# Kernel tuning notes

Measured on AMD Instinct MI355X. Metric: run time of the kernel, lower is better.

The kernel has to match this reference:

```python
import jax, jax.numpy as jnp
import numpy as np

HEADS = 16
KV_HEADS = 4
DIM_HEAD = 128
DIM = 2048
ROPE_BASE = 10000.0


def rotate_half(t):
    t1, t2 = jnp.split(t, 2, axis=-1)
    return jnp.concatenate((-t2, t1), axis=-1)


def apply_rotary(t, cos, sin):
    # t: [b, h, n, d]; cos/sin: [n, d]
    return t * cos + rotate_half(t) * sin


def setup_inputs() -> dict:
    key = jax.random.key(0)
    ks = jax.random.split(key, 6)
    b, n = 4, 1024
    s = 1.0 / np.sqrt(DIM)
    x = jax.random.normal(ks[0], (b, n, DIM), dtype=jnp.float32)
    Wq = jax.random.normal(ks[1], (DIM, HEADS * DIM_HEAD), dtype=jnp.float32) * s
    Wk = jax.random.normal(ks[2], (DIM, KV_HEADS * DIM_HEAD), dtype=jnp.float32) * s
    Wv = jax.random.normal(ks[3], (DIM, KV_HEADS * DIM_HEAD), dtype=jnp.float32) * s
    Wo = jax.random.normal(ks[4], (HEADS * DIM_HEAD, DIM), dtype=jnp.float32) * s
    head_scale = 1.0 + 0.02 * jax.random.normal(ks[5], (1, HEADS, 1, 1), dtype=jnp.float32)
    return {"x": x, "Wq": Wq, "Wk": Wk, "Wv": Wv, "Wo": Wo, "head_scale": head_scale}


def reference(x, Wq, Wk, Wv, Wo, head_scale):
    b, n, _ = x.shape
    # projections
    q = (x @ Wq).reshape(b, n, HEADS, DIM_HEAD).transpose(0, 2, 1, 3)      # b h n d
    k = (x @ Wk).reshape(b, n, KV_HEADS, DIM_HEAD).transpose(0, 2, 1, 3)   # b kv n d
    v = (x @ Wv).reshape(b, n, KV_HEADS, DIM_HEAD).transpose(0, 2, 1, 3)
    # rotary embeddings
    inv_freq = 1.0 / (ROPE_BASE ** (jnp.arange(0, DIM_HEAD, 2, dtype=jnp.float32) / DIM_HEAD))
    freqs = jnp.arange(n, dtype=jnp.float32)[:, None] * inv_freq[None, :]  # n, d/2
    emb = jnp.concatenate((freqs, freqs), axis=-1)                          # n, d
    cos, sin = jnp.cos(emb), jnp.sin(emb)
    q = apply_rotary(q, cos, sin)
    k = apply_rotary(k, cos, sin)
    # GQA: expand kv heads to query heads
    rep = HEADS // KV_HEADS
    k = jnp.repeat(k, rep, axis=1)
    v = jnp.repeat(v, rep, axis=1)
    # attention with causal mask
    scale = 1.0 / jnp.sqrt(jnp.array(DIM_HEAD, dtype=x.dtype))
    scores = jnp.einsum('bhid,bhjd->bhij', q, k) * scale
    causal = jnp.tril(jnp.ones((n, n), dtype=bool))
    scores = jnp.where(causal, scores, jnp.finfo(scores.dtype).min)
    attn = jax.nn.softmax(scores, axis=-1)
    out = jnp.einsum('bhij,bhjd->bhid', attn, v)
    out = out * head_scale                                                  # learned per-head scale
    out = out.transpose(0, 2, 1, 3).reshape(b, n, HEADS * DIM_HEAD)
    return out @ Wo
```

## Files before the change

kernel.cpp:

```cpp
#include <hip/hip_runtime.h>

typedef __attribute__((ext_vector_type(8))) short short8;
typedef __attribute__((ext_vector_type(8), may_alias)) short short8a;
typedef __attribute__((ext_vector_type(4))) short short4a_ __attribute__((may_alias));
typedef __attribute__((ext_vector_type(4))) float float4_;
typedef __attribute__((ext_vector_type(4), may_alias)) float float4a;

__device__ __forceinline__ float b2f(short h) {
  unsigned int u = ((unsigned int)(unsigned short)h) << 16;
  return __builtin_bit_cast(float, u);
}
__device__ __forceinline__ short f2b(float f) {
  unsigned int u = __builtin_bit_cast(unsigned int, f);
  u += 0x7fffu + ((u >> 16) & 1u);
  return (short)(unsigned short)(u >> 16);
}

#define GLOBAL_AS __attribute__((address_space(1)))
#define LDS_AS    __attribute__((address_space(3)))
__device__ __forceinline__ void async_copy16(void* lds, const void* g) {
  __builtin_amdgcn_global_load_lds((GLOBAL_AS const void*)g, (LDS_AS void*)lds, 16, 0, 0);
}

__global__ __launch_bounds__(256) void prep(const float* __restrict__ x,
                                            const float* __restrict__ Wq,
                                            const float* __restrict__ Wk,
                                            const float* __restrict__ Wv,
                                            const float* __restrict__ Wo,
                                            short* __restrict__ xb,
                                            short* __restrict__ wqkvt,
                                            short* __restrict__ wot) {
  __shared__ float tile[64][65];
  int bid = blockIdx.x;
  if (bid < 1536) {
    int k0 = (bid & 31) * 64, n0 = (bid >> 5) * 64;
    for (int idx = threadIdx.x; idx < 4096; idx += 256) {
      int r = idx >> 6, cc = idx & 63;
      int n = n0 + cc;
      float v;
      if (n < 2048)      v = Wq[(size_t)(k0 + r) * 2048 + n];
      else if (n < 2560) v = Wk[(size_t)(k0 + r) * 512 + (n - 2048)];
      else               v = Wv[(size_t)(k0 + r) * 512 + (n - 2560)];
      tile[r][cc] = v;
    }
    __syncthreads();
    for (int idx = threadIdx.x; idx < 4096; idx += 256) {
      int r = idx >> 6, cc = idx & 63;
      wqkvt[(size_t)(n0 + r) * 2048 + k0 + cc] = f2b(tile[cc][r]);
    }
  } else if (bid < 2560) {
    int t = bid - 1536;
    int k0 = (t & 31) * 64, n0 = (t >> 5) * 64;
    for (int idx = threadIdx.x; idx < 4096; idx += 256) {
      int r = idx >> 6, cc = idx & 63;
      tile[r][cc] = Wo[(size_t)(k0 + r) * 2048 + n0 + cc];
    }
    __syncthreads();
    for (int idx = threadIdx.x; idx < 4096; idx += 256) {
      int r = idx >> 6, cc = idx & 63;
      wot[(size_t)(n0 + r) * 2048 + k0 + cc] = f2b(tile[cc][r]);
    }
  } else {
    int i = (bid - 2560) * 256 + threadIdx.x;
    float4a v = ((const float4a*)x)[i];
    short4a_ o;
    o.x = f2b(v.x); o.y = f2b(v.y); o.z = f2b(v.z); o.w = f2b(v.w);
    ((short4a_*)xb)[i] = o;
  }
}

template <bool BF16OUT>
__global__ __launch_bounds__(256, 2)
void gemm_bt(const short* __restrict__ A, const short* __restrict__ B,
             void* __restrict__ Cv, int M, int N, int K) {
  __shared__ alignas(16) short lA[128 * 64];
  __shared__ alignas(16) short lB[128 * 64];
  const int tid = threadIdx.x;
  const int wave = tid >> 6, lane = tid & 63;
  const int quad = lane >> 4, l16 = lane & 15;
  const int m0 = blockIdx.x * 128, n0 = blockIdx.y * 128;
  const int wm = (wave >> 1) * 64, wn = (wave & 1) * 64;
  float4_ acc[4][4];
#pragma unroll
  for (int i = 0; i < 4; i++)
#pragma unroll
    for (int j = 0; j < 4; j++) acc[i][j] = (float4_){0.f, 0.f, 0.f, 0.f};
  const int nK = K >> 6;
  const int srow = lane >> 3, slot = lane & 7;
  for (int kt = 0; kt < nK; ++kt) {
    __syncthreads();
#pragma unroll
    for (int cth = 0; cth < 4; ++cth) {
      int rb = wave * 32 + cth * 8;
      int r = rb + srow;
      int c = slot ^ (r & 7);
      async_copy16(&lA[rb * 64], A + (size_t)(m0 + r) * K + kt * 64 + c * 8);
      async_copy16(&lB[rb * 64], B + (size_t)(n0 + r) * K + kt * 64 + c * 8);
    }
    __syncthreads();
#pragma unroll
    for (int kc = 0; kc < 2; ++kc) {
      short8 af[4], bf[4];
      int cch = kc * 4 + quad;
#pragma unroll
      for (int mt = 0; mt < 4; ++mt) {
        int ar = wm + mt * 16 + l16;
        af[mt] = *(const short8a*)&lA[ar * 64 + (cch ^ (ar & 7)) * 8];
      }
#pragma unroll
      for (int nt = 0; nt < 4; ++nt) {
        int br = wn + nt * 16 + l16;
        bf[nt] = *(const short8a*)&lB[br * 64 + (cch ^ (br & 7)) * 8];
      }
#pragma unroll
      for (int mt = 0; mt < 4; ++mt)
#pragma unroll
        for (int nt = 0; nt < 4; ++nt)
          acc[mt][nt] = __builtin_amdgcn_mfma_f32_16x16x32_bf16(af[mt], bf[nt], acc[mt][nt], 0, 0, 0);
    }
  }
#pragma unroll
  for (int mt = 0; mt < 4; ++mt)
#pragma unroll
    for (int nt = 0; nt < 4; ++nt) {
      int row = m0 + wm + mt * 16 + quad * 4;
      int col = n0 + wn + nt * 16 + l16;
      float4_ v = acc[mt][nt];
      if (BF16OUT) {
        short* Cb = (short*)Cv;
#pragma unroll
        for (int r = 0; r < 4; r++) Cb[(size_t)(row + r) * N + col] = f2b(v[r]);
      } else {
        float* Cf = (float*)Cv;
#pragma unroll
        for (int r = 0; r < 4; r++) Cf[(size_t)(row + r) * N + col] = v[r];
      }
    }
}

__global__ __launch_bounds__(256) void rope(short* __restrict__ qkv) {
  __shared__ float cs[64], sn[64];
  int row = blockIdx.x;
  int pos = row & 1023;
  if (threadIdx.x < 64) {
    float inv = exp2f((float)threadIdx.x * -0.20762050593478f);
    float a = (float)pos * inv;
    cs[threadIdx.x] = cosf(a);
    sn[threadIdx.x] = sinf(a);
  }
  __syncthreads();
  short* p = qkv + (size_t)row * 3072;
  for (int t = threadIdx.x; t < 1280; t += 256) {
    int hh = t >> 6, i = t & 63;
    int base = (hh < 16) ? hh * 128 : 2048 + (hh - 16) * 128;
    float scl = (hh < 16) ? 0.08838834764831845f : 1.0f;
    float c = cs[i], s = sn[i];
    float t1 = b2f(p[base + i]), t2 = b2f(p[base + 64 + i]);
    p[base + i]      = f2b((t1 * c - t2 * s) * scl);
    p[base + 64 + i] = f2b((t2 * c + t1 * s) * scl);
  }
}

__global__ __launch_bounds__(256) void vt_build(const short* __restrict__ qkv, short* __restrict__ vt) {
  __shared__ short tile[128][65];
  int bkv = blockIdx.x, n0 = blockIdx.y * 64;
  int b = bkv >> 2, kv = bkv & 3;
  const short* src = qkv + (size_t)(b * 1024) * 3072 + 2560 + kv * 128;
#pragma unroll
  for (int it = 0; it < 4; ++it) {
    int n = it * 16 + (threadIdx.x >> 4), ch = threadIdx.x & 15;
    short8a v = *(const short8a*)(src + (size_t)(n0 + n) * 3072 + ch * 8);
#pragma unroll
    for (int j = 0; j < 8; ++j) tile[ch * 8 + j][n] = v[j];
  }
  __syncthreads();
#pragma unroll
  for (int it = 0; it < 4; ++it) {
    int idx = it * 256 + threadIdx.x;
    int d = idx >> 3, ch = idx & 7;
    short8a v;
#pragma unroll
    for (int j = 0; j < 8; ++j) v[j] = tile[d][ch * 8 + j];
    *(short8a*)(vt + (size_t)(bkv * 128 + d) * 1024 + n0 + ch * 8) = v;
  }
}

__global__ __launch_bounds__(256, 2)
void flash(const short* __restrict__ qkv, const short* __restrict__ vt,
           const float* __restrict__ head_scale, short* __restrict__ attn) {
  __shared__ alignas(16) short lK[64 * 128];
  __shared__ alignas(16) short lV[128 * 64];
  __shared__ alignas(16) short lP[4][16 * 72];
  const int tid = threadIdx.x, wave = tid >> 6, lane = tid & 63;
  const int quad = lane >> 4, l16 = lane & 15;
  const int bh = blockIdx.x, b = bh >> 4, h = bh & 15, kv = h >> 2;
  const int qt = (gridDim.y - 1) - blockIdx.y;
  short8 qf[4];
  {
    int qrow = qt * 64 + wave * 16 + l16;
    const short* qp = qkv + (size_t)(b * 1024 + qrow) * 3072 + h * 128;
#pragma unroll
    for (int kc = 0; kc < 4; kc++) qf[kc] = *(const short8a*)(qp + kc * 32 + quad * 8);
  }
  float4_ O[8];
#pragma unroll
  for (int i = 0; i < 8; i++) O[i] = (float4_){0.f, 0.f, 0.f, 0.f};
  float rsacc[4] = {0.f, 0.f, 0.f, 0.f};
  const size_t kbase = (size_t)(b * 1024) * 3072 + 2048 + kv * 128;
  const size_t vbase = (size_t)((b * 4 + kv) * 128) * 1024;
  const int slot16 = lane & 15, rr4 = lane >> 4;
  const int slot8 = lane & 7, dr8 = lane >> 3;
  for (int kt = 0; kt <= qt; ++kt) {
    __syncthreads();
#pragma unroll
    for (int cc = 0; cc < 4; ++cc) {
      int rb = wave * 16 + cc * 4;
      int r = rb + rr4;
      int c = slot16 ^ (r & 15);
      async_copy16(&lK[rb * 128], qkv + kbase + (size_t)(kt * 64 + r) * 3072 + c * 8);
    }
#pragma unroll
    for (int cc = 0; cc < 4; ++cc) {
      int db = wave * 32 + cc * 8;
      int d = db + dr8;
      int c = slot8 ^ (d & 7);
      async_copy16(&lV[db * 64], vt + vbase + (size_t)d * 1024 + kt * 64 + c * 8);
    }
    __syncthreads();
    float4_ S[4];
#pragma unroll
    for (int st = 0; st < 4; ++st) {
      float4_ s = (float4_){0.f, 0.f, 0.f, 0.f};
      int kr = st * 16 + l16;
#pragma unroll
      for (int kc = 0; kc < 4; ++kc) {
        int c = kc * 4 + quad;
        short8 kf = *(const short8a*)&lK[kr * 128 + (c ^ (kr & 15)) * 8];
        s = __builtin_amdgcn_mfma_f32_16x16x32_bf16(qf[kc], kf, s, 0, 0, 0);
      }
      S[st] = s;
    }
    if (kt == qt) {
#pragma unroll
      for (int st = 0; st < 4; ++st)
#pragma unroll
        for (int r = 0; r < 4; r++)
          if (st * 16 + l16 > wave * 16 + quad * 4 + r) S[st][r] = -1e30f;
    }
#pragma unroll
    for (int st = 0; st < 4; ++st)
#pragma unroll
      for (int r = 0; r < 4; r++) {
        float pv = __expf(S[st][r]);
        rsacc[r] += pv;
        lP[wave][(quad * 4 + r) * 72 + st * 16 + l16] = f2b(pv);
      }
    short8 pf[2];
#pragma unroll
    for (int kc2 = 0; kc2 < 2; kc2++)
      pf[kc2] = *(const short8a*)&lP[wave][l16 * 72 + kc2 * 32 + quad * 8];
#pragma unroll
    for (int dt = 0; dt < 8; ++dt) {
      int d = dt * 16 + l16;
#pragma unroll
      for (int kc2 = 0; kc2 < 2; kc2++) {
        int c = kc2 * 4 + quad;
        short8 vf = *(const short8a*)&lV[d * 64 + (c ^ (d & 7)) * 8];
        O[dt] = __builtin_amdgcn_mfma_f32_16x16x32_bf16(pf[kc2], vf, O[dt], 0, 0, 0);
      }
    }
  }
  float l_i[4];
#pragma unroll
  for (int r = 0; r < 4; r++) {
    float rs = rsacc[r];
#pragma unroll
    for (int off = 8; off; off >>= 1) rs += __shfl_xor(rs, off, 64);
    l_i[r] = rs;
  }
  float hs = head_scale[h];
  int qrow = qt * 64 + wave * 16 + quad * 4;
#pragma unroll
  for (int dt = 0; dt < 8; ++dt) {
    int col = h * 128 + dt * 16 + l16;
#pragma unroll
    for (int r = 0; r < 4; r++) {
      float o = O[dt][r] * (hs / l_i[r]);
      attn[(size_t)(b * 1024 + qrow + r) * 2048 + col] = f2b(o);
    }
  }
}

extern "C" void kernel_launch(void* const* d_in, const int* in_sizes, int n_in,
                              void* d_out, int out_size, void* d_ws, size_t ws_size,
                              hipStream_t stream) {
  const float* x  = (const float*)d_in[0];
  const float* Wq = (const float*)d_in[1];
  const float* Wk = (const float*)d_in[2];
  const float* Wv = (const float*)d_in[3];
  const float* Wo = (const float*)d_in[4];
  const float* hs = (const float*)d_in[5];
  float* out = (float*)d_out;
  char* ws = (char*)d_ws;
  short* xb    = (short*)(ws);
  short* wqkvt = (short*)(ws + 16777216);
  short* wot   = (short*)(ws + 29360128);
  short* qkv   = (short*)(ws + 37748736);
  short* vt    = (short*)(ws + 62914560);
  short* attn  = xb;

  prep<<<10752, 256, 0, stream>>>(x, Wq, Wk, Wv, Wo, xb, wqkvt, wot);
  gemm_bt<true><<<dim3(32, 24), 256, 0, stream>>>(xb, wqkvt, (void*)qkv, 4096, 3072, 2048);
  rope<<<4096, 256, 0, stream>>>(qkv);
  vt_build<<<dim3(16, 16), 256, 0, stream>>>(qkv, vt);
  flash<<<dim3(64, 16), 256, 0, stream>>>(qkv, vt, hs, attn);
  gemm_bt<false><<<dim3(32, 16), 256, 0, stream>>>(attn, wot, (void*)out, 4096, 2048, 2048);
}
```

Baseline: 253.3 us.

## Fuse RoPE into QKV GEMM epilogue and process 128-row query tiles in flash

Measured after the change: 256.8 us. No clear change (+1.4%).

```diff
diff --git a/kernel.cpp b/kernel.cpp
--- a/kernel.cpp
+++ b/kernel.cpp
@@ -3,6 +3,7 @@
 typedef __attribute__((ext_vector_type(8))) short short8;
 typedef __attribute__((ext_vector_type(8), may_alias)) short short8a;
 typedef __attribute__((ext_vector_type(4))) short short4a_ __attribute__((may_alias));
+typedef __attribute__((ext_vector_type(2), may_alias)) short short2a;
 typedef __attribute__((ext_vector_type(4))) float float4_;
 typedef __attribute__((ext_vector_type(4), may_alias)) float float4a;
 
@@ -38,7 +39,7 @@
       int r = idx >> 6, cc = idx & 63;
       int n = n0 + cc;
       float v;
-      if (n < 2048)      v = Wq[(size_t)(k0 + r) * 2048 + n];
+      if (n < 2048)      v = Wq[(size_t)(k0 + r) * 2048 + n] * 0.08838834764831845f;
       else if (n < 2560) v = Wk[(size_t)(k0 + r) * 512 + (n - 2048)];
       else               v = Wv[(size_t)(k0 + r) * 512 + (n - 2560)];
       tile[r][cc] = v;
@@ -69,12 +70,13 @@
   }
 }
 
-template <bool BF16OUT>
+template <int MODE>
 __global__ __launch_bounds__(256, 2)
 void gemm_bt(const short* __restrict__ A, const short* __restrict__ B,
              void* __restrict__ Cv, int M, int N, int K) {
-  __shared__ alignas(16) short lA[128 * 64];
-  __shared__ alignas(16) short lB[128 * 64];
+  __shared__ alignas(16) short lsm[MODE == 1 ? 16896 : 16384];
+  short* lA = lsm;
+  short* lB = lsm + 8192;
   const int tid = threadIdx.x;
   const int wave = tid >> 6, lane = tid & 63;
   const int quad = lane >> 4, l16 = lane & 15;
@@ -119,45 +121,55 @@
           acc[mt][nt] = __builtin_amdgcn_mfma_f32_16x16x32_bf16(af[mt], bf[nt], acc[mt][nt], 0, 0, 0);
     }
   }
-#pragma unroll
-  for (int mt = 0; mt < 4; ++mt)
-#pragma unroll
-    for (int nt = 0; nt < 4; ++nt) {
-      int row = m0 + wm + mt * 16 + quad * 4;
-      int col = n0 + wn + nt * 16 + l16;
-      float4_ v = acc[mt][nt];
-      if (BF16OUT) {
-        short* Cb = (short*)Cv;
-#pragma unroll
-        for (int r = 0; r < 4; r++) Cb[(size_t)(row + r) * N + col] = f2b(v[r]);
-      } else {
-        float* Cf = (float*)Cv;
-#pragma unroll
-        for (int r = 0; r < 4; r++) Cf[(size_t)(row + r) * N + col] = v[r];
-      }
-    }
-}
-
-__global__ __launch_bounds__(256) void rope(short* __restrict__ qkv) {
-  __shared__ float cs[64], sn[64];
-  int row = blockIdx.x;
-  int pos = row & 1023;
-  if (threadIdx.x < 64) {
-    float inv = exp2f((float)threadIdx.x * -0.20762050593478f);
-    float a = (float)pos * inv;
-    cs[threadIdx.x] = cosf(a);
-    sn[threadIdx.x] = sinf(a);
-  }
-  __syncthreads();
-  short* p = qkv + (size_t)row * 3072;
-  for (int t = threadIdx.x; t < 1280; t += 256) {
-    int hh = t >> 6, i = t & 63;
-    int base = (hh < 16) ? hh * 128 : 2048 + (hh - 16) * 128;
-    float scl = (hh < 16) ? 0.08838834764831845f : 1.0f;
-    float c = cs[i], s = sn[i];
-    float t1 = b2f(p[base + i]), t2 = b2f(p[base + 64 + i]);
-    p[base + i]      = f2b((t1 * c - t2 * s) * scl);
-    p[base + 64 + i] = f2b((t2 * c + t1 * s) * scl);
+  if (MODE == 1 && n0 < 2560) {
+    __syncthreads();
+    short* lC = lsm;
+#pragma unroll
+    for (int mt = 0; mt < 4; ++mt)
+#pragma unroll
+      for (int nt = 0; nt < 4; ++nt)
+#pragma unroll
+        for (int r = 0; r < 4; r++)
+          lC[(wm + mt * 16 + quad * 4 + r) * 132 + wn + nt * 16 + l16] = f2b(acc[mt][nt][r]);
+    __syncthreads();
+    short* Cb = (short*)Cv;
+    const int posBase = m0 & 1023;
+#pragma unroll
+    for (int it = 0; it < 16; ++it) {
+      int idx = it * 256 + tid;
+      int row = idx >> 5;
+      int c2 = (idx & 31) * 2;
+      float t1a = b2f(lC[row * 132 + c2]),      t1b = b2f(lC[row * 132 + c2 + 1]);
+      float t2a = b2f(lC[row * 132 + c2 + 64]), t2b = b2f(lC[row * 132 + c2 + 65]);
+      float pos = (float)(posBase + row);
+      float sa, ca, sb, cb;
+      sincosf(pos * exp2f((float)c2 * -0.20762050593478f), &sa, &ca);
+      sincosf(pos * exp2f((float)(c2 + 1) * -0.20762050593478f), &sb, &cb);
+      short2a o1, o2;
+      o1.x = f2b(t1a * ca - t2a * sa); o1.y = f2b(t1b * cb - t2b * sb);
+      o2.x = f2b(t2a * ca + t1a * sa); o2.y = f2b(t2b * cb + t1b * sb);
+      size_t base = (size_t)(m0 + row) * N + n0;
+      *(short2a*)&Cb[base + c2] = o1;
+      *(short2a*)&Cb[base + c2 + 64] = o2;
+    }
+  } else {
+#pragma unroll
+    for (int mt = 0; mt < 4; ++mt)
+#pragma unroll
+      for (int nt = 0; nt < 4; ++nt) {
+        int row = m0 + wm + mt * 16 + quad * 4;
+        int col = n0 + wn + nt * 16 + l16;
+        float4_ v = acc[mt][nt];
+        if (MODE == 1) {
+          short* Cb = (short*)Cv;
+#pragma unroll
+          for (int r = 0; r < 4; r++) Cb[(size_t)(row + r) * N + col] = f2b(v[r]);
+        } else {
+          float* Cf = (float*)Cv;
+#pragma unroll
+          for (int r = 0; r < 4; r++) Cf[(size_t)(row + r) * N + col] = v[r];
+        }
+      }
   }
 }
 
@@ -190,27 +202,32 @@
            const float* __restrict__ head_scale, short* __restrict__ attn) {
   __shared__ alignas(16) short lK[64 * 128];
   __shared__ alignas(16) short lV[128 * 64];
-  __shared__ alignas(16) short lP[4][16 * 72];
+  __shared__ alignas(16) short lP[4][32 * 72];
   const int tid = threadIdx.x, wave = tid >> 6, lane = tid & 63;
   const int quad = lane >> 4, l16 = lane & 15;
   const int bh = blockIdx.x, b = bh >> 4, h = bh & 15, kv = h >> 2;
-  const int qt = (gridDim.y - 1) - blockIdx.y;
-  short8 qf[4];
-  {
-    int qrow = qt * 64 + wave * 16 + l16;
+  const int qt = 7 - blockIdx.y;
+  const int base_w = qt * 128 + wave * 32;
+  short8 qf[2][4];
+#pragma unroll
+  for (int g = 0; g < 2; g++) {
+    int qrow = base_w + g * 16 + l16;
     const short* qp = qkv + (size_t)(b * 1024 + qrow) * 3072 + h * 128;
 #pragma unroll
-    for (int kc = 0; kc < 4; kc++) qf[kc] = *(const short8a*)(qp + kc * 32 + quad * 8);
-  }
-  float4_ O[8];
-#pragma unroll
-  for (int i = 0; i < 8; i++) O[i] = (float4_){0.f, 0.f, 0.f, 0.f};
-  float rsacc[4] = {0.f, 0.f, 0.f, 0.f};
+    for (int kc = 0; kc < 4; kc++) qf[g][kc] = *(const short8a*)(qp + kc * 32 + quad * 8);
+  }
+  float4_ O[2][8];
+#pragma unroll
+  for (int g = 0; g < 2; g++)
+#pragma unroll
+    for (int i = 0; i < 8; i++) O[g][i] = (float4_){0.f, 0.f, 0.f, 0.f};
+  float rsacc[2][4] = {{0.f, 0.f, 0.f, 0.f}, {0.f, 0.f, 0.f, 0.f}};
   const size_t kbase = (size_t)(b * 1024) * 3072 + 2048 + kv * 128;
   const size_t vbase = (size_t)((b * 4 + kv) * 128) * 1024;
   const int slot16 = lane & 15, rr4 = lane >> 4;
   const int slot8 = lane & 7, dr8 = lane >> 3;
-  for (int kt = 0; kt <= qt; ++kt) {
+  const int nkt = 2 * qt + 2;
+  for (int kt = 0; kt < nkt; ++kt) {
     __syncthreads();
 #pragma unroll
     for (int cc = 0; cc < 4; ++cc) {
@@ -227,38 +244,46 @@
       async_copy16(&lV[db * 64], vt + vbase + (size_t)d * 1024 + kt * 64 + c * 8);
     }
     __syncthreads();
-    float4_ S[4];
+    if (kt * 64 > base_w + 31) continue;
+    float4_ S[2][4];
 #pragma unroll
     for (int st = 0; st < 4; ++st) {
-      float4_ s = (float4_){0.f, 0.f, 0.f, 0.f};
+      float4_ s0 = (float4_){0.f, 0.f, 0.f, 0.f}, s1 = s0;
       int kr = st * 16 + l16;
 #pragma unroll
       for (int kc = 0; kc < 4; ++kc) {
         int c = kc * 4 + quad;
         short8 kf = *(const short8a*)&lK[kr * 128 + (c ^ (kr & 15)) * 8];
-        s = __builtin_amdgcn_mfma_f32_16x16x32_bf16(qf[kc], kf, s, 0, 0, 0);
-      }
-      S[st] = s;
-    }
-    if (kt == qt) {
+        s0 = __builtin_amdgcn_mfma_f32_16x16x32_bf16(qf[0][kc], kf, s0, 0, 0, 0);
+        s1 = __builtin_amdgcn_mfma_f32_16x16x32_bf16(qf[1][kc], kf, s1, 0, 0, 0);
+      }
+      S[0][st] = s0; S[1][st] = s1;
+    }
+#pragma unroll
+    for (int g = 0; g < 2; g++) {
+      int gbase = base_w + g * 16;
+      if (kt * 64 + 63 > gbase) {
+#pragma unroll
+        for (int st = 0; st < 4; ++st)
+#pragma unroll
+          for (int r = 0; r < 4; r++)
+            if (kt * 64 + st * 16 + l16 > gbase + quad * 4 + r) S[g][st][r] = -1e30f;
+      }
 #pragma unroll
       for (int st = 0; st < 4; ++st)
 #pragma unroll
-        for (int r = 0; r < 4; r++)
-          if (st * 16 + l16 > wave * 16 + quad * 4 + r) S[st][r] = -1e30f;
-    }
-#pragma unroll
-    for (int st = 0; st < 4; ++st)
-#pragma unroll
-      for (int r = 0; r < 4; r++) {
-        float pv = __expf(S[st][r]);
-        rsacc[r] += pv;
-        lP[wave][(quad * 4 + r) * 72 + st * 16 + l16] = f2b(pv);
-      }
-    short8 pf[2];
-#pragma unroll
-    for (int kc2 = 0; kc2 < 2; kc2++)
-      pf[kc2] = *(const short8a*)&lP[wave][l16 * 72 + kc2 * 32 + quad * 8];
+        for (int r = 0; r < 4; r++) {
+          float pv = __expf(S[g][st][r]);
+          rsacc[g][r] += pv;
+          lP[wave][(g * 16 + quad * 4 + r) * 72 + st * 16 + l16] = f2b(pv);
+        }
+    }
+    short8 pf[2][2];
+#pragma unroll
+    for (int g = 0; g < 2; g++)
+#pragma unroll
+      for (int kc2 = 0; kc2 < 2; kc2++)
+        pf[g][kc2] = *(const short8a*)&lP[wave][(g * 16 + l16) * 72 + kc2 * 32 + quad * 8];
 #pragma unroll
     for (int dt = 0; dt < 8; ++dt) {
       int d = dt * 16 + l16;
@@ -266,27 +291,31 @@
       for (int kc2 = 0; kc2 < 2; kc2++) {
         int c = kc2 * 4 + quad;
         short8 vf = *(const short8a*)&lV[d * 64 + (c ^ (d & 7)) * 8];
-        O[dt] = __builtin_amdgcn_mfma_f32_16x16x32_bf16(pf[kc2], vf, O[dt], 0, 0, 0);
-      }
-    }
-  }
-  float l_i[4];
-#pragma unroll
-  for (int r = 0; r < 4; r++) {
-    float rs = rsacc[r];
-#pragma unroll
-    for (int off = 8; off; off >>= 1) rs += __shfl_xor(rs, off, 64);
-    l_i[r] = rs;
+        O[0][dt] = __builtin_amdgcn_mfma_f32_16x16x32_bf16(pf[0][kc2], vf, O[0][dt], 0, 0, 0);
+        O[1][dt] = __builtin_amdgcn_mfma_f32_16x16x32_bf16(pf[1][kc2], vf, O[1][dt], 0, 0, 0);
+      }
+    }
   }
   float hs = head_scale[h];
-  int qrow = qt * 64 + wave * 16 + quad * 4;
-#pragma unroll
-  for (int dt = 0; dt < 8; ++dt) {
-    int col = h * 128 + dt * 16 + l16;
+#pragma unroll
+  for (int g = 0; g < 2; g++) {
+    float l_i[4];
 #pragma unroll
     for (int r = 0; r < 4; r++) {
-      float o = O[dt][r] * (hs / l_i[r]);
-      attn[(size_t)(b * 1024 + qrow + r) * 2048 + col] = f2b(o);
+      float rs = rsacc[g][r];
+#pragma unroll
+      for (int off = 8; off; off >>= 1) rs += __shfl_xor(rs, off, 64);
+      l_i[r] = rs;
+    }
+    int qrow = base_w + g * 16 + quad * 4;
+#pragma unroll
+    for (int dt = 0; dt < 8; ++dt) {
+      int col = h * 128 + dt * 16 + l16;
+#pragma unroll
+      for (int r = 0; r < 4; r++) {
+        float o = O[g][dt][r] * (hs / l_i[r]);
+        attn[(size_t)(b * 1024 + qrow + r) * 2048 + col] = f2b(o);
+      }
     }
   }
 }
@@ -310,9 +339,8 @@
   short* attn  = xb;
 
   prep<<<10752, 256, 0, stream>>>(x, Wq, Wk, Wv, Wo, xb, wqkvt, wot);
-  gemm_bt<true><<<dim3(32, 24), 256, 0, stream>>>(xb, wqkvt, (void*)qkv, 4096, 3072, 2048);
-  rope<<<4096, 256, 0, stream>>>(qkv);
+  gemm_bt<1><<<dim3(32, 24), 256, 0, stream>>>(xb, wqkvt, (void*)qkv, 4096, 3072, 2048);
   vt_build<<<dim3(16, 16), 256, 0, stream>>>(qkv, vt);
-  flash<<<dim3(64, 16), 256, 0, stream>>>(qkv, vt, hs, attn);
-  gemm_bt<false><<<dim3(32, 16), 256, 0, stream>>>(attn, wot, (void*)out, 4096, 2048, 2048);
-}
+  flash<<<dim3(64, 8), 256, 0, stream>>>(qkv, vt, hs, attn);
+  gemm_bt<0><<<dim3(32, 16), 256, 0, stream>>>(attn, wot, (void*)out, 4096, 2048, 2048);
+}
```
